# Optimization experiments

Hardware: AMD Instinct MI355X
Metric: run time of the kernel (lower is better)

The kernel has to match this reference:

```python
import jax, jax.numpy as jnp
import numpy as np

EMBED_DIM = 1024
NUM_HEADS = 16
HEAD_DIM = EMBED_DIM // NUM_HEADS


def setup_inputs() -> dict:
    key = jax.random.key(0)
    k1, k2, k3 = jax.random.split(key, 3)
    B, T = 2, 2048
    query = jax.random.normal(k1, (B, T, EMBED_DIM), dtype=jnp.float32)
    # xavier_uniform_ for Linear(embed_dim, 3*embed_dim): limit = sqrt(6/(fan_in+fan_out))
    lim_qkv = float(np.sqrt(6.0 / (EMBED_DIM + 3 * EMBED_DIM)))
    Wqkv = jax.random.uniform(k2, (3 * EMBED_DIM, EMBED_DIM), dtype=jnp.float32,
                              minval=-lim_qkv, maxval=lim_qkv)
    bqkv = jnp.zeros((3 * EMBED_DIM,), dtype=jnp.float32)
    lim_o = float(np.sqrt(6.0 / (EMBED_DIM + EMBED_DIM)))
    Wo = jax.random.uniform(k3, (EMBED_DIM, EMBED_DIM), dtype=jnp.float32,
                            minval=-lim_o, maxval=lim_o)
    bo = jnp.zeros((EMBED_DIM,), dtype=jnp.float32)
    return {"query": query, "Wqkv": Wqkv, "bqkv": bqkv, "Wo": Wo, "bo": bo}


def reference(query, Wqkv, bqkv, Wo, bo):
    B, T, E = query.shape
    H, D = NUM_HEADS, HEAD_DIM
    scaling = D ** -0.5
    # fused qkv projection from `query` (original ignores key/value tensors)
    qkv = jnp.einsum('bte,fe->btf', query, Wqkv) + bqkv  # [B, T, 3E]
    q, k, v = jnp.split(qkv, 3, axis=-1)
    # [B, H, T, D]
    q = q.reshape(B, T, H, D).transpose(0, 2, 1, 3) * scaling
    k = k.reshape(B, T, H, D).transpose(0, 2, 1, 3)
    v = v.reshape(B, T, H, D).transpose(0, 2, 1, 3)
    scores = jnp.einsum('bhtd,bhsd->bhts', q, k)          # [B, H, T, T]
    attn = jax.nn.softmax(scores, axis=-1)
    out = jnp.einsum('bhts,bhsd->bhtd', attn, v)           # [B, H, T, D]
    out = out.transpose(0, 2, 1, 3).reshape(B, T, E)
    out = jnp.einsum('bte,fe->btf', out, Wo) + bo
    return out
```

## Files before the change

kernel.cpp:

```cpp
#include <hip/hip_runtime.h>
#include <hip/hip_bf16.h>

#define B_ 2
#define T_ 2048
#define E_ 1024
#define H_ 16
#define D_ 64
#define F_ 3072
#define M_ 4096
#define VT_STRIDE 2080
#define QSCALE 0.1803368801111f
#define THR_LOG2 11.5f

typedef __attribute__((ext_vector_type(8))) short short8v;
typedef __attribute__((ext_vector_type(4))) float float4v;

#if __has_builtin(__builtin_amdgcn_exp2f)
#define EXP2(x) __builtin_amdgcn_exp2f(x)
#else
#define EXP2(x) exp2f(x)
#endif

__device__ __forceinline__ unsigned cvtpk(float lo, float hi) {
    union { __hip_bfloat162 h; unsigned u; } x;
    x.h = __float22bfloat162_rn(float2{lo, hi});
    return x.u;
}
__device__ __forceinline__ ushort f2bf(float f) { return (ushort)cvtpk(f, f); }

__global__ void cvt_kernel(const float* __restrict__ in, ushort* __restrict__ out, int n4) {
    int i = blockIdx.x * blockDim.x + threadIdx.x;
    if (i >= n4) return;
    float4 v = ((const float4*)in)[i];
    uint2 o;
    o.x = cvtpk(v.x, v.y);
    o.y = cvtpk(v.z, v.w);
    ((uint2*)out)[i] = o;
}

template <int MODE>
__global__ __launch_bounds__(256) void gemm_bt(const ushort* __restrict__ A,
                                               const ushort* __restrict__ Bt,
                                               const float* __restrict__ bias,
                                               void* __restrict__ Cout,
                                               int Ndim, int K) {
    __shared__ __attribute__((aligned(16))) char lds[32768];
    int t = threadIdx.x;
    int lane = t & 63;
    int w = t >> 6;
    int wr = w >> 1, wc = w & 1;
    int bm0 = blockIdx.x * 128, bn0 = blockIdx.y * 128;
    int mb = bm0 + wr * 64;
    int nb = bn0 + wc * 64;
    int r15 = lane & 15, g = lane >> 4;

    int srow = w * 8 + (lane >> 3);
    int schunk = (lane & 7) ^ (lane >> 3);
    const ushort* Asrc = A + (size_t)(bm0 + srow) * K + schunk * 8;
    const ushort* Bsrc = Bt + (size_t)(bn0 + srow) * K + schunk * 8;

    int rxor7 = r15 & 7;
    int abase = (wr * 64 + r15) * 128;
    int bbase = 16384 + (wc * 64 + r15) * 128;

    float4v acc[4][4] = {};
    for (int k0 = 0; k0 < K; k0 += 64) {
#pragma unroll
        for (int j = 0; j < 4; ++j) {
            __builtin_amdgcn_global_load_lds(
                (const __attribute__((address_space(1))) void*)(Asrc + (size_t)(j * 32) * K + k0),
                (__attribute__((address_space(3))) void*)(lds + j * 4096 + w * 1024),
                16, 0, 0);
            __builtin_amdgcn_global_load_lds(
                (const __attribute__((address_space(1))) void*)(Bsrc + (size_t)(j * 32) * K + k0),
                (__attribute__((address_space(3))) void*)(lds + 16384 + j * 4096 + w * 1024),
                16, 0, 0);
        }
        __syncthreads();

        short8v af[4][2], bf[4][2];
#pragma unroll
        for (int r = 0; r < 4; ++r)
#pragma unroll
            for (int h = 0; h < 2; ++h)
                af[r][h] = *(const short8v*)(lds + abase + r * 2048 +
                                             (((h * 4 + g) ^ rxor7) << 4));
#pragma unroll
        for (int c = 0; c < 4; ++c)
#pragma unroll
            for (int h = 0; h < 2; ++h)
                bf[c][h] = *(const short8v*)(lds + bbase + c * 2048 +
                                             (((h * 4 + g) ^ rxor7) << 4));
#pragma unroll
        for (int r = 0; r < 4; ++r)
#pragma unroll
            for (int c = 0; c < 4; ++c) {
                acc[r][c] = __builtin_amdgcn_mfma_f32_16x16x32_bf16(af[r][0], bf[c][0], acc[r][c], 0, 0, 0);
                acc[r][c] = __builtin_amdgcn_mfma_f32_16x16x32_bf16(af[r][1], bf[c][1], acc[r][c], 0, 0, 0);
            }
        __syncthreads();
    }

    if (MODE == 0) {
        ushort* qkv = (ushort*)Cout;
#pragma unroll
        for (int r = 0; r < 4; ++r)
#pragma unroll
            for (int c = 0; c < 4; ++c)
#pragma unroll
                for (int ri = 0; ri < 4; ++ri) {
                    int m = mb + r * 16 + g * 4 + ri;
                    int n = nb + c * 16 + r15;
                    float v = acc[r][c][ri] + bias[n];
                    int which = n >> 10;
                    int e = n & 1023;
                    if (which == 0) v *= QSCALE;
                    int h = e >> 6, d = e & 63;
                    int b = m >> 11, tt0 = m & 2047;
                    size_t addr;
                    if (which == 2) {
                        int tt = tt0 & 63;
                        int c64 = ((tt >> 2) & 3) * 16 + (tt >> 4) * 4 + (tt & 3);
                        int tp = (tt0 & ~63) | c64;
                        addr = (size_t)2 * M_ * E_ +
                               ((size_t)(b * H_ + h) * D_ + d) * VT_STRIDE + tp;
                    } else {
                        addr = (size_t)which * M_ * E_ +
                               ((size_t)(b * H_ + h) * T_ + tt0) * D_ + d;
                    }
                    qkv[addr] = f2bf(v);
                }
    } else {
        float* out = (float*)Cout;
#pragma unroll
        for (int r = 0; r < 4; ++r)
#pragma unroll
            for (int c = 0; c < 4; ++c)
#pragma unroll
                for (int ri = 0; ri < 4; ++ri) {
                    int m = mb + r * 16 + g * 4 + ri;
                    int n = nb + c * 16 + r15;
                    out[(size_t)m * Ndim + n] = acc[r][c][ri] + bias[n];
                }
    }
}

__global__ __launch_bounds__(256, 2) void attn_kernel(const ushort* __restrict__ qkv,
                                                      ushort* __restrict__ Ob) {
    int lane = threadIdx.x & 63;
    int w = threadIdx.x >> 6;
    int bid = blockIdx.x;
    int slot = bid >> 3;
    int bh = (bid & 7) * 4 + (slot >> 4);
    int qt = slot & 15;
    int r15 = lane & 15, g = lane >> 4;
    int qb = qt * 128 + w * 32;

    const ushort* Qh = qkv + (size_t)bh * T_ * D_;
    const ushort* Kh = qkv + (size_t)M_ * E_ + (size_t)bh * T_ * D_;
    const ushort* Vt = qkv + (size_t)2 * M_ * E_ + (size_t)bh * D_ * VT_STRIDE;

    const ushort* QrowA = Qh + (size_t)(qb + r15) * D_ + g * 8;
    short8v qfA0 = *(const short8v*)(QrowA);
    short8v qfA1 = *(const short8v*)(QrowA + 32);
    short8v qfB0 = *(const short8v*)(QrowA + 16 * D_);
    short8v qfB1 = *(const short8v*)(QrowA + 16 * D_ + 32);

    float4v oaccA[4] = {}, oaccB[4] = {};
    float mA = -1e30f, lA = 0.f;
    float mB = -1e30f, lB = 0.f;

    const ushort* Kp0 = Kh + (size_t)r15 * D_ + g * 8;
    const ushort* vr0 = Vt + (size_t)(0 * 16 + r15) * VT_STRIDE + g * 16;
    const ushort* vr1 = Vt + (size_t)(1 * 16 + r15) * VT_STRIDE + g * 16;
    const ushort* vr2 = Vt + (size_t)(2 * 16 + r15) * VT_STRIDE + g * 16;
    const ushort* vr3 = Vt + (size_t)(3 * 16 + r15) * VT_STRIDE + g * 16;

    struct KT  { short8v r0a, r0b, r1a, r1b, r2a, r2b, r3a, r3b; };
    struct VTl { short8v c00, c01, c10, c11, c20, c21, c30, c31; };

    auto loadK = [&](int kt) {
        const ushort* p = Kp0 + (size_t)kt * 64 * D_;
        KT t;
        t.r0a = *(const short8v*)(p);            t.r0b = *(const short8v*)(p + 32);
        t.r1a = *(const short8v*)(p + 16 * D_);  t.r1b = *(const short8v*)(p + 16 * D_ + 32);
        t.r2a = *(const short8v*)(p + 32 * D_);  t.r2b = *(const short8v*)(p + 32 * D_ + 32);
        t.r3a = *(const short8v*)(p + 48 * D_);  t.r3b = *(const short8v*)(p + 48 * D_ + 32);
        return t;
    };
    auto loadV = [&](int kt) {
        int off = kt * 64;
        VTl t;
        t.c00 = *(const short8v*)(vr0 + off); t.c01 = *(const short8v*)(vr0 + off + 8);
        t.c10 = *(const short8v*)(vr1 + off); t.c11 = *(const short8v*)(vr1 + off + 8);
        t.c20 = *(const short8v*)(vr2 + off); t.c21 = *(const short8v*)(vr2 + off + 8);
        t.c30 = *(const short8v*)(vr3 + off); t.c31 = *(const short8v*)(vr3 + off + 8);
        return t;
    };

    auto softmax64 = [&](const float4v& s0, const float4v& s1, const float4v& s2,
                         const float4v& s3, float& m_run, float& l_run,
                         float4v* oacc, short8v& pf0, short8v& pf1) {
        float t0 = fmaxf(fmaxf(s0[0], s0[1]), fmaxf(s0[2], s0[3]));
        float t1 = fmaxf(fmaxf(s1[0], s1[1]), fmaxf(s1[2], s1[3]));
        float t2 = fmaxf(fmaxf(s2[0], s2[1]), fmaxf(s2[2], s2[3]));
        float t3 = fmaxf(fmaxf(s3[0], s3[1]), fmaxf(s3[2], s3[3]));
        float tmax = fmaxf(fmaxf(t0, t1), fmaxf(t2, t3));
        if (!__all(tmax - m_run <= THR_LOG2)) {
            float tr = fmaxf(tmax, __shfl_xor(tmax, 16));
            tr = fmaxf(tr, __shfl_xor(tr, 32));
            float mnew = fmaxf(m_run, tr);
            float corr = EXP2(m_run - mnew);
            float c0 = __shfl(corr, g * 4 + 0);
            float c1 = __shfl(corr, g * 4 + 1);
            float c2 = __shfl(corr, g * 4 + 2);
            float c3 = __shfl(corr, g * 4 + 3);
#pragma unroll
            for (int c = 0; c < 4; ++c) {
                oacc[c][0] *= c0; oacc[c][1] *= c1;
                oacc[c][2] *= c2; oacc[c][3] *= c3;
            }
            l_run *= corr;
            m_run = mnew;
        }
        float p0 = EXP2(s0[0] - m_run), p1 = EXP2(s0[1] - m_run);
        float p2 = EXP2(s0[2] - m_run), p3 = EXP2(s0[3] - m_run);
        float p4 = EXP2(s1[0] - m_run), p5 = EXP2(s1[1] - m_run);
        float p6 = EXP2(s1[2] - m_run), p7 = EXP2(s1[3] - m_run);
        float p8 = EXP2(s2[0] - m_run), p9 = EXP2(s2[1] - m_run);
        float pa = EXP2(s2[2] - m_run), pb = EXP2(s2[3] - m_run);
        float pc = EXP2(s3[0] - m_run), pd = EXP2(s3[1] - m_run);
        float pe = EXP2(s3[2] - m_run), pg = EXP2(s3[3] - m_run);
        l_run += (((p0 + p1) + (p2 + p3)) + ((p4 + p5) + (p6 + p7))) +
                 (((p8 + p9) + (pa + pb)) + ((pc + pd) + (pe + pg)));
        union { short8v v; unsigned u[4]; } u0, u1;
        u0.u[0] = cvtpk(p0, p1); u0.u[1] = cvtpk(p2, p3);
        u0.u[2] = cvtpk(p4, p5); u0.u[3] = cvtpk(p6, p7);
        u1.u[0] = cvtpk(p8, p9); u1.u[1] = cvtpk(pa, pb);
        u1.u[2] = cvtpk(pc, pd); u1.u[3] = cvtpk(pe, pg);
        pf0 = u0.v; pf1 = u1.v;
    };

    auto process = [&](const KT& K, const VTl& V) {
        float4v sA0 = {}, sA1 = {}, sA2 = {}, sA3 = {};
        float4v sB0 = {}, sB1 = {}, sB2 = {}, sB3 = {};
        __builtin_amdgcn_s_setprio(1);
        sA0 = __builtin_amdgcn_mfma_f32_16x16x32_bf16(K.r0a, qfA0, sA0, 0, 0, 0);
        sA0 = __builtin_amdgcn_mfma_f32_16x16x32_bf16(K.r0b, qfA1, sA0, 0, 0, 0);
        sA1 = __builtin_amdgcn_mfma_f32_16x16x32_bf16(K.r1a, qfA0, sA1, 0, 0, 0);
        sA1 = __builtin_amdgcn_mfma_f32_16x16x32_bf16(K.r1b, qfA1, sA1, 0, 0, 0);
        sA2 = __builtin_amdgcn_mfma_f32_16x16x32_bf16(K.r2a, qfA0, sA2, 0, 0, 0);
        sA2 = __builtin_amdgcn_mfma_f32_16x16x32_bf16(K.r2b, qfA1, sA2, 0, 0, 0);
        sA3 = __builtin_amdgcn_mfma_f32_16x16x32_bf16(K.r3a, qfA0, sA3, 0, 0, 0);
        sA3 = __builtin_amdgcn_mfma_f32_16x16x32_bf16(K.r3b, qfA1, sA3, 0, 0, 0);
        sB0 = __builtin_amdgcn_mfma_f32_16x16x32_bf16(K.r0a, qfB0, sB0, 0, 0, 0);
        sB0 = __builtin_amdgcn_mfma_f32_16x16x32_bf16(K.r0b, qfB1, sB0, 0, 0, 0);
        sB1 = __builtin_amdgcn_mfma_f32_16x16x32_bf16(K.r1a, qfB0, sB1, 0, 0, 0);
        sB1 = __builtin_amdgcn_mfma_f32_16x16x32_bf16(K.r1b, qfB1, sB1, 0, 0, 0);
        sB2 = __builtin_amdgcn_mfma_f32_16x16x32_bf16(K.r2a, qfB0, sB2, 0, 0, 0);
        sB2 = __builtin_amdgcn_mfma_f32_16x16x32_bf16(K.r2b, qfB1, sB2, 0, 0, 0);
        sB3 = __builtin_amdgcn_mfma_f32_16x16x32_bf16(K.r3a, qfB0, sB3, 0, 0, 0);
        sB3 = __builtin_amdgcn_mfma_f32_16x16x32_bf16(K.r3b, qfB1, sB3, 0, 0, 0);
        __builtin_amdgcn_s_setprio(0);

        short8v pA0, pA1, pB0, pB1;
        softmax64(sA0, sA1, sA2, sA3, mA, lA, oaccA, pA0, pA1);
        softmax64(sB0, sB1, sB2, sB3, mB, lB, oaccB, pB0, pB1);

        __builtin_amdgcn_s_setprio(1);
        oaccA[0] = __builtin_amdgcn_mfma_f32_16x16x32_bf16(pA0, V.c00, oaccA[0], 0, 0, 0);
        oaccA[0] = __builtin_amdgcn_mfma_f32_16x16x32_bf16(pA1, V.c01, oaccA[0], 0, 0, 0);
        oaccB[0] = __builtin_amdgcn_mfma_f32_16x16x32_bf16(pB0, V.c00, oaccB[0], 0, 0, 0);
        oaccB[0] = __builtin_amdgcn_mfma_f32_16x16x32_bf16(pB1, V.c01, oaccB[0], 0, 0, 0);
        oaccA[1] = __builtin_amdgcn_mfma_f32_16x16x32_bf16(pA0, V.c10, oaccA[1], 0, 0, 0);
        oaccA[1] = __builtin_amdgcn_mfma_f32_16x16x32_bf16(pA1, V.c11, oaccA[1], 0, 0, 0);
        oaccB[1] = __builtin_amdgcn_mfma_f32_16x16x32_bf16(pB0, V.c10, oaccB[1], 0, 0, 0);
        oaccB[1] = __builtin_amdgcn_mfma_f32_16x16x32_bf16(pB1, V.c11, oaccB[1], 0, 0, 0);
        oaccA[2] = __builtin_amdgcn_mfma_f32_16x16x32_bf16(pA0, V.c20, oaccA[2], 0, 0, 0);
        oaccA[2] = __builtin_amdgcn_mfma_f32_16x16x32_bf16(pA1, V.c21, oaccA[2], 0, 0, 0);
        oaccB[2] = __builtin_amdgcn_mfma_f32_16x16x32_bf16(pB0, V.c20, oaccB[2], 0, 0, 0);
        oaccB[2] = __builtin_amdgcn_mfma_f32_16x16x32_bf16(pB1, V.c21, oaccB[2], 0, 0, 0);
        oaccA[3] = __builtin_amdgcn_mfma_f32_16x16x32_bf16(pA0, V.c30, oaccA[3], 0, 0, 0);
        oaccA[3] = __builtin_amdgcn_mfma_f32_16x16x32_bf16(pA1, V.c31, oaccA[3], 0, 0, 0);
        oaccB[3] = __builtin_amdgcn_mfma_f32_16x16x32_bf16(pB0, V.c30, oaccB[3], 0, 0, 0);
        oaccB[3] = __builtin_amdgcn_mfma_f32_16x16x32_bf16(pB1, V.c31, oaccB[3], 0, 0, 0);
        __builtin_amdgcn_s_setprio(0);
    };

    KT  kc = loadK(0);
    VTl vc = loadV(0);
    for (int kt = 0; kt < T_ / 64; kt += 2) {
        KT  kn = loadK(kt + 1);
        VTl vn = loadV(kt + 1);
        process(kc, vc);
        if (kt + 2 < T_ / 64) {
            kc = loadK(kt + 2);
            vc = loadV(kt + 2);
        }
        process(kn, vn);
    }

    lA += __shfl_xor(lA, 16); lA += __shfl_xor(lA, 32);
    lB += __shfl_xor(lB, 16); lB += __shfl_xor(lB, 32);

    int b = bh >> 4, h = bh & 15;
    {
        float i0 = 1.f / __shfl(lA, g * 4 + 0), i1 = 1.f / __shfl(lA, g * 4 + 1);
        float i2 = 1.f / __shfl(lA, g * 4 + 2), i3 = 1.f / __shfl(lA, g * 4 + 3);
#pragma unroll
        for (int c = 0; c < 4; ++c) {
            size_t base = ((size_t)b * T_ + qb + g * 4) * E_ + h * 64 + c * 16 + r15;
            Ob[base]          = f2bf(oaccA[c][0] * i0);
            Ob[base + E_]     = f2bf(oaccA[c][1] * i1);
            Ob[base + 2 * E_] = f2bf(oaccA[c][2] * i2);
            Ob[base + 3 * E_] = f2bf(oaccA[c][3] * i3);
        }
    }
    {
        float i0 = 1.f / __shfl(lB, g * 4 + 0), i1 = 1.f / __shfl(lB, g * 4 + 1);
        float i2 = 1.f / __shfl(lB, g * 4 + 2), i3 = 1.f / __shfl(lB, g * 4 + 3);
#pragma unroll
        for (int c = 0; c < 4; ++c) {
            size_t base = ((size_t)b * T_ + qb + 16 + g * 4) * E_ + h * 64 + c * 16 + r15;
            Ob[base]          = f2bf(oaccB[c][0] * i0);
            Ob[base + E_]     = f2bf(oaccB[c][1] * i1);
            Ob[base + 2 * E_] = f2bf(oaccB[c][2] * i2);
            Ob[base + 3 * E_] = f2bf(oaccB[c][3] * i3);
        }
    }
}

extern "C" void kernel_launch(void* const* d_in, const int* in_sizes, int n_in,
                              void* d_out, int out_size, void* d_ws, size_t ws_size,
                              hipStream_t stream) {
    const float* query = (const float*)d_in[0];
    const float* Wqkv  = (const float*)d_in[1];
    const float* bqkv  = (const float*)d_in[2];
    const float* Wo    = (const float*)d_in[3];
    const float* bo    = (const float*)d_in[4];
    float* out = (float*)d_out;

    ushort* Xb    = (ushort*)d_ws;
    ushort* Wqkvb = Xb + (size_t)M_ * E_;
    ushort* Wob   = Wqkvb + (size_t)F_ * E_;
    ushort* QKVb  = Wob + (size_t)E_ * E_;
    ushort* Ob    = Xb;

    cvt_kernel<<<(M_ * E_ / 4 + 255) / 256, 256, 0, stream>>>(query, Xb, M_ * E_ / 4);
    cvt_kernel<<<(F_ * E_ / 4 + 255) / 256, 256, 0, stream>>>(Wqkv, Wqkvb, F_ * E_ / 4);
    cvt_kernel<<<(E_ * E_ / 4 + 255) / 256, 256, 0, stream>>>(Wo, Wob, E_ * E_ / 4);

    gemm_bt<0><<<dim3(M_ / 128, F_ / 128), 256, 0, stream>>>(Xb, Wqkvb, bqkv, QKVb, F_, E_);
    attn_kernel<<<(B_ * H_) * (T_ / 128), 256, 0, stream>>>(QKVb, Ob);
    gemm_bt<1><<<dim3(M_ / 128, E_ / 128), 256, 0, stream>>>(Ob, Wob, bo, out, E_, E_);
}
```

Baseline: 238.0 us.

## Stage K/V tiles through swizzled LDS with async global_load_lds double buffering

```diff
diff --git a/kernel.cpp b/kernel.cpp
--- a/kernel.cpp
+++ b/kernel.cpp
@@ -147,8 +147,10 @@
 
 __global__ __launch_bounds__(256, 2) void attn_kernel(const ushort* __restrict__ qkv,
                                                       ushort* __restrict__ Ob) {
-    int lane = threadIdx.x & 63;
-    int w = threadIdx.x >> 6;
+    __shared__ __attribute__((aligned(16))) char lds[32768];
+    int tid = threadIdx.x;
+    int lane = tid & 63;
+    int w = tid >> 6;
     int bid = blockIdx.x;
     int slot = bid >> 3;
     int bh = (bid & 7) * 4 + (slot >> 4);
@@ -165,38 +167,40 @@
     short8v qfA1 = *(const short8v*)(QrowA + 32);
     short8v qfB0 = *(const short8v*)(QrowA + 16 * D_);
     short8v qfB1 = *(const short8v*)(QrowA + 16 * D_ + 32);
+    asm volatile("" :: "v"(qfA0), "v"(qfA1), "v"(qfB0), "v"(qfB1));
 
     float4v oaccA[4] = {}, oaccB[4] = {};
     float mA = -1e30f, lA = 0.f;
     float mB = -1e30f, lB = 0.f;
 
-    const ushort* Kp0 = Kh + (size_t)r15 * D_ + g * 8;
-    const ushort* vr0 = Vt + (size_t)(0 * 16 + r15) * VT_STRIDE + g * 16;
-    const ushort* vr1 = Vt + (size_t)(1 * 16 + r15) * VT_STRIDE + g * 16;
-    const ushort* vr2 = Vt + (size_t)(2 * 16 + r15) * VT_STRIDE + g * 16;
-    const ushort* vr3 = Vt + (size_t)(3 * 16 + r15) * VT_STRIDE + g * 16;
-
-    struct KT  { short8v r0a, r0b, r1a, r1b, r2a, r2b, r3a, r3b; };
-    struct VTl { short8v c00, c01, c10, c11, c20, c21, c30, c31; };
-
-    auto loadK = [&](int kt) {
-        const ushort* p = Kp0 + (size_t)kt * 64 * D_;
-        KT t;
-        t.r0a = *(const short8v*)(p);            t.r0b = *(const short8v*)(p + 32);
-        t.r1a = *(const short8v*)(p + 16 * D_);  t.r1b = *(const short8v*)(p + 16 * D_ + 32);
-        t.r2a = *(const short8v*)(p + 32 * D_);  t.r2b = *(const short8v*)(p + 32 * D_ + 32);
-        t.r3a = *(const short8v*)(p + 48 * D_);  t.r3b = *(const short8v*)(p + 48 * D_ + 32);
-        return t;
+    int srow = tid >> 3;
+    int slc = (tid & 7) ^ (srow & 7);
+    const ushort* Ksrc = Kh + (size_t)srow * D_ + slc * 8;
+    const ushort* Vsrc = Vt + (size_t)srow * VT_STRIDE + slc * 8;
+
+    auto stage = [&](int kt, int base) {
+        const ushort* kp = Ksrc + (size_t)kt * 64 * D_;
+        const ushort* vp = Vsrc + kt * 64;
+#pragma unroll
+        for (int i = 0; i < 2; ++i)
+            __builtin_amdgcn_global_load_lds(
+                (const __attribute__((address_space(1))) void*)(kp + (size_t)i * 32 * D_),
+                (__attribute__((address_space(3))) void*)(lds + base + i * 4096 + tid * 16),
+                16, 0, 0);
+#pragma unroll
+        for (int i = 0; i < 2; ++i)
+            __builtin_amdgcn_global_load_lds(
+                (const __attribute__((address_space(1))) void*)(vp + (size_t)i * 32 * VT_STRIDE),
+                (__attribute__((address_space(3))) void*)(lds + base + 8192 + i * 4096 + tid * 16),
+                16, 0, 0);
     };
-    auto loadV = [&](int kt) {
-        int off = kt * 64;
-        VTl t;
-        t.c00 = *(const short8v*)(vr0 + off); t.c01 = *(const short8v*)(vr0 + off + 8);
-        t.c10 = *(const short8v*)(vr1 + off); t.c11 = *(const short8v*)(vr1 + off + 8);
-        t.c20 = *(const short8v*)(vr2 + off); t.c21 = *(const short8v*)(vr2 + off + 8);
-        t.c30 = *(const short8v*)(vr3 + off); t.c31 = *(const short8v*)(vr3 + off + 8);
-        return t;
-    };
+
+    int rxor = (r15 & 7) << 4;
+    int rowb = r15 * 128;
+    int kc0 = ((g) << 4) ^ rxor;
+    int kc1 = ((g + 4) << 4) ^ rxor;
+    int vc0 = ((2 * g) << 4) ^ rxor;
+    int vc1 = ((2 * g + 1) << 4) ^ rxor;
 
     auto softmax64 = [&](const float4v& s0, const float4v& s1, const float4v& s2,
                          const float4v& s3, float& m_run, float& l_run,
@@ -241,63 +245,88 @@
         pf0 = u0.v; pf1 = u1.v;
     };
 
-    auto process = [&](const KT& K, const VTl& V) {
+    auto compute = [&](int base) {
+        const char* kb_ = lds + base;
+        const char* vb_ = lds + base + 8192;
+        short8v k0a = *(const short8v*)(kb_ + rowb + kc0);
+        short8v k0b = *(const short8v*)(kb_ + rowb + kc1);
+        short8v k1a = *(const short8v*)(kb_ + 2048 + rowb + kc0);
+        short8v k1b = *(const short8v*)(kb_ + 2048 + rowb + kc1);
+        short8v k2a = *(const short8v*)(kb_ + 4096 + rowb + kc0);
+        short8v k2b = *(const short8v*)(kb_ + 4096 + rowb + kc1);
+        short8v k3a = *(const short8v*)(kb_ + 6144 + rowb + kc0);
+        short8v k3b = *(const short8v*)(kb_ + 6144 + rowb + kc1);
+
         float4v sA0 = {}, sA1 = {}, sA2 = {}, sA3 = {};
         float4v sB0 = {}, sB1 = {}, sB2 = {}, sB3 = {};
         __builtin_amdgcn_s_setprio(1);
-        sA0 = __builtin_amdgcn_mfma_f32_16x16x32_bf16(K.r0a, qfA0, sA0, 0, 0, 0);
-        sA0 = __builtin_amdgcn_mfma_f32_16x16x32_bf16(K.r0b, qfA1, sA0, 0, 0, 0);
-        sA1 = __builtin_amdgcn_mfma_f32_16x16x32_bf16(K.r1a, qfA0, sA1, 0, 0, 0);
-        sA1 = __builtin_amdgcn_mfma_f32_16x16x32_bf16(K.r1b, qfA1, sA1, 0, 0, 0);
-        sA2 = __builtin_amdgcn_mfma_f32_16x16x32_bf16(K.r2a, qfA0, sA2, 0, 0, 0);
-        sA2 = __builtin_amdgcn_mfma_f32_16x16x32_bf16(K.r2b, qfA1, sA2, 0, 0, 0);
-        sA3 = __builtin_amdgcn_mfma_f32_16x16x32_bf16(K.r3a, qfA0, sA3, 0, 0, 0);
-        sA3 = __builtin_amdgcn_mfma_f32_16x16x32_bf16(K.r3b, qfA1, sA3, 0, 0, 0);
-        sB0 = __builtin_amdgcn_mfma_f32_16x16x32_bf16(K.r0a, qfB0, sB0, 0, 0, 0);
-        sB0 = __builtin_amdgcn_mfma_f32_16x16x32_bf16(K.r0b, qfB1, sB0, 0, 0, 0);
-        sB1 = __builtin_amdgcn_mfma_f32_16x16x32_bf16(K.r1a, qfB0, sB1, 0, 0, 0);
-        sB1 = __builtin_amdgcn_mfma_f32_16x16x32_bf16(K.r1b, qfB1, sB1, 0, 0, 0);
-        sB2 = __builtin_amdgcn_mfma_f32_16x16x32_bf16(K.r2a, qfB0, sB2, 0, 0, 0);
-        sB2 = __builtin_amdgcn_mfma_f32_16x16x32_bf16(K.r2b, qfB1, sB2, 0, 0, 0);
-        sB3 = __builtin_amdgcn_mfma_f32_16x16x32_bf16(K.r3a, qfB0, sB3, 0, 0, 0);
-        sB3 = __builtin_amdgcn_mfma_f32_16x16x32_bf16(K.r3b, qfB1, sB3, 0, 0, 0);
+        sA0 = __builtin_amdgcn_mfma_f32_16x16x32_bf16(k0a, qfA0, sA0, 0, 0, 0);
+        sA0 = __builtin_amdgcn_mfma_f32_16x16x32_bf16(k0b, qfA1, sA0, 0, 0, 0);
+        sA1 = __builtin_amdgcn_mfma_f32_16x16x32_bf16(k1a, qfA0, sA1, 0, 0, 0);
+        sA1 = __builtin_amdgcn_mfma_f32_16x16x32_bf16(k1b, qfA1, sA1, 0, 0, 0);
+        sA2 = __builtin_amdgcn_mfma_f32_16x16x32_bf16(k2a, qfA0, sA2, 0, 0, 0);
+        sA2 = __builtin_amdgcn_mfma_f32_16x16x32_bf16(k2b, qfA1, sA2, 0, 0, 0);
+        sA3 = __builtin_amdgcn_mfma_f32_16x16x32_bf16(k3a, qfA0, sA3, 0, 0, 0);
+        sA3 = __builtin_amdgcn_mfma_f32_16x16x32_bf16(k3b, qfA1, sA3, 0, 0, 0);
+        sB0 = __builtin_amdgcn_mfma_f32_16x16x32_bf16(k0a, qfB0, sB0, 0, 0, 0);
+        sB0 = __builtin_amdgcn_mfma_f32_16x16x32_bf16(k0b, qfB1, sB0, 0, 0, 0);
+        sB1 = __builtin_amdgcn_mfma_f32_16x16x32_bf16(k1a, qfB0, sB1, 0, 0, 0);
+        sB1 = __builtin_amdgcn_mfma_f32_16x16x32_bf16(k1b, qfB1, sB1, 0, 0, 0);
+        sB2 = __builtin_amdgcn_mfma_f32_16x16x32_bf16(k2a, qfB0, sB2, 0, 0, 0);
+        sB2 = __builtin_amdgcn_mfma_f32_16x16x32_bf16(k2b, qfB1, sB2, 0, 0, 0);
+        sB3 = __builtin_amdgcn_mfma_f32_16x16x32_bf16(k3a, qfB0, sB3, 0, 0, 0);
+        sB3 = __builtin_amdgcn_mfma_f32_16x16x32_bf16(k3b, qfB1, sB3, 0, 0, 0);
         __builtin_amdgcn_s_setprio(0);
+
+        short8v v0a = *(const short8v*)(vb_ + rowb + vc0);
+        short8v v0b = *(const short8v*)(vb_ + rowb + vc1);
+        short8v v1a = *(const short8v*)(vb_ + 2048 + rowb + vc0);
+        short8v v1b = *(const short8v*)(vb_ + 2048 + rowb + vc1);
+        short8v v2a = *(const short8v*)(vb_ + 4096 + rowb + vc0);
+        short8v v2b = *(const short8v*)(vb_ + 4096 + rowb + vc1);
+        short8v v3a = *(const short8v*)(vb_ + 6144 + rowb + vc0);
+        short8v v3b = *(const short8v*)(vb_ + 6144 + rowb + vc1);
 
         short8v pA0, pA1, pB0, pB1;
         softmax64(sA0, sA1, sA2, sA3, mA, lA, oaccA, pA0, pA1);
         softmax64(sB0, sB1, sB2, sB3, mB, lB, oaccB, pB0, pB1);
 
         __builtin_amdgcn_s_setprio(1);
-        oaccA[0] = __builtin_amdgcn_mfma_f32_16x16x32_bf16(pA0, V.c00, oaccA[0], 0, 0, 0);
-        oaccA[0] = __builtin_amdgcn_mfma_f32_16x16x32_bf16(pA1, V.c01, oaccA[0], 0, 0, 0);
-        oaccB[0] = __builtin_amdgcn_mfma_f32_16x16x32_bf16(pB0, V.c00, oaccB[0], 0, 0, 0);
-        oaccB[0] = __builtin_amdgcn_mfma_f32_16x16x32_bf16(pB1, V.c01, oaccB[0], 0, 0, 0);
-        oaccA[1] = __builtin_amdgcn_mfma_f32_16x16x32_bf16(pA0, V.c10, oaccA[1], 0, 0, 0);
-        oaccA[1] = __builtin_amdgcn_mfma_f32_16x16x32_bf16(pA1, V.c11, oaccA[1], 0, 0, 0);
-        oaccB[1] = __builtin_amdgcn_mfma_f32_16x16x32_bf16(pB0, V.c10, oaccB[1], 0, 0, 0);
-        oaccB[1] = __builtin_amdgcn_mfma_f32_16x16x32_bf16(pB1, V.c11, oaccB[1], 0, 0, 0);
-        oaccA[2] = __builtin_amdgcn_mfma_f32_16x16x32_bf16(pA0, V.c20, oaccA[2], 0, 0, 0);
-        oaccA[2] = __builtin_amdgcn_mfma_f32_16x16x32_bf16(pA1, V.c21, oaccA[2], 0, 0, 0);
-        oaccB[2] = __builtin_amdgcn_mfma_f32_16x16x32_bf16(pB0, V.c20, oaccB[2], 0, 0, 0);
-        oaccB[2] = __builtin_amdgcn_mfma_f32_16x16x32_bf16(pB1, V.c21, oaccB[2], 0, 0, 0);
-        oaccA[3] = __builtin_amdgcn_mfma_f32_16x16x32_bf16(pA0, V.c30, oaccA[3], 0, 0, 0);
-        oaccA[3] = __builtin_amdgcn_mfma_f32_16x16x32_bf16(pA1, V.c31, oaccA[3], 0, 0, 0);
-        oaccB[3] = __builtin_amdgcn_mfma_f32_16x16x32_bf16(pB0, V.c30, oaccB[3], 0, 0, 0);
-        oaccB[3] = __builtin_amdgcn_mfma_f32_16x16x32_bf16(pB1, V.c31, oaccB[3], 0, 0, 0);
+        oaccA[0] = __builtin_amdgcn_mfma_f32_16x16x32_bf16(pA0, v0a, oaccA[0], 0, 0, 0);
+        oaccA[0] = __builtin_amdgcn_mfma_f32_16x16x32_bf16(pA1, v0b, oaccA[0], 0, 0, 0);
+        oaccB[0] = __builtin_amdgcn_mfma_f32_16x16x32_bf16(pB0, v0a, oaccB[0], 0, 0, 0);
+        oaccB[0] = __builtin_amdgcn_mfma_f32_16x16x32_bf16(pB1, v0b, oaccB[0], 0, 0, 0);
+        oaccA[1] = __builtin_amdgcn_mfma_f32_16x16x32_bf16(pA0, v1a, oaccA[1], 0, 0, 0);
+        oaccA[1] = __builtin_amdgcn_mfma_f32_16x16x32_bf16(pA1, v1b, oaccA[1], 0, 0, 0);
+        oaccB[1] = __builtin_amdgcn_mfma_f32_16x16x32_bf16(pB0, v1a, oaccB[1], 0, 0, 0);
+        oaccB[1] = __builtin_amdgcn_mfma_f32_16x16x32_bf16(pB1, v1b, oaccB[1], 0, 0, 0);
+        oaccA[2] = __builtin_amdgcn_mfma_f32_16x16x32_bf16(pA0, v2a, oaccA[2], 0, 0, 0);
+        oaccA[2] = __builtin_amdgcn_mfma_f32_16x16x32_bf16(pA1, v2b, oaccA[2], 0, 0, 0);
+        oaccB[2] = __builtin_amdgcn_mfma_f32_16x16x32_bf16(pB0, v2a, oaccB[2], 0, 0, 0);
+        oaccB[2] = __builtin_amdgcn_mfma_f32_16x16x32_bf16(pB1, v2b, oaccB[2], 0, 0, 0);
+        oaccA[3] = __builtin_amdgcn_mfma_f32_16x16x32_bf16(pA0, v3a, oaccA[3], 0, 0, 0);
+        oaccA[3] = __builtin_amdgcn_mfma_f32_16x16x32_bf16(pA1, v3b, oaccA[3], 0, 0, 0);
+        oaccB[3] = __builtin_amdgcn_mfma_f32_16x16x32_bf16(pB0, v3a, oaccB[3], 0, 0, 0);
+        oaccB[3] = __builtin_amdgcn_mfma_f32_16x16x32_bf16(pB1, v3b, oaccB[3], 0, 0, 0);
         __builtin_amdgcn_s_setprio(0);
     };
 
-    KT  kc = loadK(0);
-    VTl vc = loadV(0);
+    stage(0, 0);
     for (int kt = 0; kt < T_ / 64; kt += 2) {
-        KT  kn = loadK(kt + 1);
-        VTl vn = loadV(kt + 1);
-        process(kc, vc);
+        stage(kt + 1, 16384);
+        asm volatile("s_waitcnt vmcnt(4)" ::: "memory");
+        __builtin_amdgcn_s_barrier();
+        compute(0);
+        __builtin_amdgcn_s_barrier();
         if (kt + 2 < T_ / 64) {
-            kc = loadK(kt + 2);
-            vc = loadV(kt + 2);
-        }
-        process(kn, vn);
+            stage(kt + 2, 0);
+            asm volatile("s_waitcnt vmcnt(4)" ::: "memory");
+        } else {
+            asm volatile("s_waitcnt vmcnt(0)" ::: "memory");
+        }
+        __builtin_amdgcn_s_barrier();
+        compute(16384);
+        __builtin_amdgcn_s_barrier();
     }
 
     lA += __shfl_xor(lA, 16); lA += __shfl_xor(lA, 32);
```

New measurement: 197.1 us. 1.21x faster.
